# Optimization experiments

Measured on AMD Instinct MI355X. Metric: run time of the kernel, lower is better.

Reference implementation:

```python
import jax, jax.numpy as jnp
import numpy as np
import math

B, C, F, W = 2, 8, 512, 1024
HEADS = 8


def _mcl(x, Wm, b):
    # per-channel linear over feature dim: x (b,c,g,w), Wm (c,f,g), b (c,f)
    return jnp.einsum('bcgw,cfg->bcfw', x, Wm) + b[None, :, :, None]


def _conv(x, w, b, pad):
    y = jax.lax.conv_general_dilated(
        x, w, window_strides=(1, 1), padding=[(0, 0), (pad, pad)],
        dimension_numbers=('NCHW', 'OIHW', 'NCHW'))
    return y + b[None, :, None, None]


def _rope(t):
    # t: (..., seq, d); lucidrains-style interleaved rotary
    d = t.shape[-1]
    seq = t.shape[-2]
    inv_freq = 1.0 / (10000.0 ** (jnp.arange(0, d, 2, dtype=jnp.float32) / d))
    freqs = jnp.arange(seq, dtype=jnp.float32)[:, None] * inv_freq[None, :]  # (seq, d/2)
    emb = jnp.repeat(freqs, 2, axis=-1)  # (seq, d), interleaved f0,f0,f1,f1,...
    cos, sin = jnp.cos(emb), jnp.sin(emb)
    tp = t.reshape(t.shape[:-1] + (d // 2, 2))
    rot = jnp.stack([-tp[..., 1], tp[..., 0]], axis=-1).reshape(t.shape)
    return t * cos.astype(t.dtype) + rot * sin.astype(t.dtype)


def setup_inputs() -> dict:
    key = jax.random.key(0)
    ks = jax.random.split(key, 18)
    s = 0.02
    d = {'x': jax.random.normal(ks[0], (B, C, F, W), dtype=jnp.float32)}
    names = ['q', 'k', 'v', 'o']
    for i, n in enumerate(names):
        d['W' + n] = jax.random.normal(ks[1 + 4 * i], (C, F, F), dtype=jnp.float32) * s
        d['b' + n] = jnp.zeros((C, F), dtype=jnp.float32)
        kw = 7 if n != 'o' else 1
        d[n + '_conv_w'] = jax.random.normal(ks[2 + 4 * i], (C, C, 1, kw), dtype=jnp.float32) * s
        d[n + '_conv_b'] = jnp.zeros((C,), dtype=jnp.float32)
    return d


def reference(x, Wq, bq, q_conv_w, q_conv_b, Wk, bk, k_conv_w, k_conv_b,
              Wv, bv, v_conv_w, v_conv_b, Wo, bo, o_conv_w, o_conv_b):
    b, c, h, w = x.shape
    dh = h // HEADS

    def split_heads(y):  # (b,c,h,w) -> (b,c,heads,w,dh)
        return y.transpose(0, 1, 3, 2).reshape(b, c, w, HEADS, dh).transpose(0, 1, 3, 2, 4)

    q = _rope(split_heads(_conv(_mcl(x, Wq, bq), q_conv_w, q_conv_b, 3)))
    k = _rope(split_heads(_conv(_mcl(x, Wk, bk), k_conv_w, k_conv_b, 3)))
    v = split_heads(_conv(_mcl(x, Wv, bv), v_conv_w, v_conv_b, 3))

    # forced fp32 attention, scaled by sqrt(h) = sqrt(features)
    qk = jnp.einsum('bceqd,bcekd->bceqk', q.astype(jnp.float32), k.astype(jnp.float32)) / math.sqrt(h)
    a = jax.nn.softmax(qk, axis=-1)
    o = jnp.einsum('bceqk,bcekd->bceqd', a, v.astype(jnp.float32))  # (b,c,heads,w,dh)
    o = o.transpose(0, 1, 3, 2, 4).reshape(b, c, w, h).transpose(0, 1, 3, 2)  # (b,c,h,w)

    return _conv(_mcl(o, Wo, bo), o_conv_w, o_conv_b, 0)
```

## Files before the change

kernel.cpp:

```cpp
#include <hip/hip_runtime.h>
#include <hip/hip_bf16.h>
#include <math.h>

#define W_ 1024
#define F_ 512
#define C_ 8
#define B_ 2
#define DH_ 64

typedef __attribute__((ext_vector_type(8))) short short8;
typedef __attribute__((ext_vector_type(4))) short short4v;
typedef __attribute__((ext_vector_type(4))) float f32x4;

__device__ inline unsigned short f2bf(float x) {
    union { float f; unsigned u; } v; v.f = x;
    unsigned r = v.u + 0x7fff + ((v.u >> 16) & 1);
    return (unsigned short)(r >> 16);
}
__device__ inline float bf2f(unsigned short x) {
    union { unsigned u; float f; } v; v.u = (unsigned)x << 16; return v.f;
}

__device__ inline void gll16(const void* g, void* l) {
    __builtin_amdgcn_global_load_lds(
        (const __attribute__((address_space(1))) unsigned int*)g,
        (__attribute__((address_space(3))) unsigned int*)l, 16, 0, 0);
}

__global__ __launch_bounds__(256) void rope_table_kernel(float* __restrict__ cost,
                                                         float* __restrict__ sint) {
    int idx = blockIdx.x * 256 + threadIdx.x;
    if (idx >= W_ * 32) return;
    int w = idx >> 5, i = idx & 31;
    double freq = pow(10000.0, -(double)(2 * i) / 64.0);
    double ang = (double)w * freq;
    cost[idx] = (float)cos(ang);
    sint[idx] = (float)sin(ang);
}

__global__ __launch_bounds__(256) void xt_kernel(
    const float* __restrict__ In, unsigned short* __restrict__ Out)
{
    const int wt = blockIdx.x;
    const int gc = blockIdx.y;
    const int bc = blockIdx.z;
    __shared__ unsigned short T[128][72];
    const int t = threadIdx.x;
    const float* src = In + (size_t)bc * F_ * W_ + (size_t)gc * 64 * W_ + wt * 128;
    const int d0 = (t >> 4) * 4;
    const int w0 = (t & 15) * 4;
    #pragma unroll
    for (int it = 0; it < 2; ++it) {
        int wbase = w0 + it * 64;
        float4 row[4];
        #pragma unroll
        for (int k = 0; k < 4; ++k)
            row[k] = *(const float4*)(src + (size_t)(d0 + k) * W_ + wbase);
        #pragma unroll
        for (int wp = 0; wp < 4; ++wp) {
            ushort4 p;
            p.x = f2bf(((const float*)&row[0])[wp]);
            p.y = f2bf(((const float*)&row[1])[wp]);
            p.z = f2bf(((const float*)&row[2])[wp]);
            p.w = f2bf(((const float*)&row[3])[wp]);
            *(ushort4*)&T[wbase + wp][d0] = p;
        }
    }
    __syncthreads();
    unsigned short* dst = Out + (size_t)bc * W_ * F_ + (size_t)(wt * 128) * F_ + gc * 64;
    const int w = t >> 1, hf = (t & 1) * 32;
    const unsigned short* sr = &T[w][hf];
    uint4* dr = (uint4*)(dst + (size_t)w * F_ + hf);
    dr[0] = ((const uint4*)sr)[0];
    dr[1] = ((const uint4*)sr)[1];
    dr[2] = ((const uint4*)sr)[2];
    dr[3] = ((const uint4*)sr)[3];
}

template<int BF16OUT>
__device__ inline void mcl_body(const unsigned short* Ag, const unsigned short* Bg,
                                const float* biasp, float* Cp, unsigned short* CpB,
                                int f0, int w0)
{
    __shared__ unsigned short As_[128 * 64];
    __shared__ unsigned short Bs_[128 * 64];
    __shared__ float scr[4][16 * 17];

    const int t = threadIdx.x;
    const int wid = t >> 6, lane = t & 63;
    const int l15 = lane & 15, l4 = lane >> 4;
    const int wf = wid >> 1, ww = wid & 1;

    const int grow = lane >> 3;
    const int gcol = ((lane & 7) * 16) ^ ((grow & 7) << 4);

    f32x4 acc[4][4];
    #pragma unroll
    for (int mt = 0; mt < 4; ++mt)
        #pragma unroll
        for (int nt = 0; nt < 4; ++nt) acc[mt][nt] = (f32x4){0.f, 0.f, 0.f, 0.f};

    for (int ks = 0; ks < 8; ++ks) {
        const int k0 = ks * 64;
        __syncthreads();
        #pragma unroll
        for (int i = 0; i < 4; ++i) {
            int rbase = wid * 32 + i * 8;
            int row = rbase + grow;
            gll16(Ag + (size_t)(f0 + row) * F_ + k0 + (gcol >> 1), &As_[rbase * 64]);
            gll16(Bg + (size_t)(w0 + row) * F_ + k0 + (gcol >> 1), &Bs_[rbase * 64]);
        }
        __syncthreads();
        #pragma unroll
        for (int kf = 0; kf < 2; ++kf) {
            short8 af[4], bf_[4];
            #pragma unroll
            for (int mt = 0; mt < 4; ++mt) {
                int row = wf * 64 + mt * 16 + l15;
                int off = (kf * 64 + l4 * 16) ^ ((row & 7) << 4);
                af[mt] = *(const short8*)((const char*)As_ + row * 128 + off);
            }
            #pragma unroll
            for (int nt = 0; nt < 4; ++nt) {
                int row = ww * 64 + nt * 16 + l15;
                int off = (kf * 64 + l4 * 16) ^ ((row & 7) << 4);
                bf_[nt] = *(const short8*)((const char*)Bs_ + row * 128 + off);
            }
            #pragma unroll
            for (int mt = 0; mt < 4; ++mt)
                #pragma unroll
                for (int nt = 0; nt < 4; ++nt)
                    acc[mt][nt] = __builtin_amdgcn_mfma_f32_16x16x32_bf16(af[mt], bf_[nt], acc[mt][nt], 0, 0, 0);
        }
    }

    const float* bp = biasp + f0 + wf * 64;
    float bz[4][4];
    #pragma unroll
    for (int mt = 0; mt < 4; ++mt)
        #pragma unroll
        for (int r = 0; r < 4; ++r) bz[mt][r] = bp[mt * 16 + l4 * 4 + r];

    float* sw = scr[wid];
    #pragma unroll
    for (int mt = 0; mt < 4; ++mt)
        #pragma unroll
        for (int nt = 0; nt < 4; ++nt) {
            #pragma unroll
            for (int r = 0; r < 4; ++r)
                sw[(l4 * 4 + r) * 17 + l15] = acc[mt][nt][r] + bz[mt][r];
            float4 o;
            o.x = sw[l15 * 17 + l4 * 4 + 0];
            o.y = sw[l15 * 17 + l4 * 4 + 1];
            o.z = sw[l15 * 17 + l4 * 4 + 2];
            o.w = sw[l15 * 17 + l4 * 4 + 3];
            size_t off = (size_t)(f0 + wf * 64 + mt * 16 + l15) * W_
                       + w0 + ww * 64 + nt * 16 + l4 * 4;
            if (BF16OUT) {
                ushort4 p;
                p.x = f2bf(o.x); p.y = f2bf(o.y); p.z = f2bf(o.z); p.w = f2bf(o.w);
                *(ushort4*)(CpB + off) = p;
            } else {
                *(float4*)(Cp + off) = o;
            }
        }
}

__global__ __launch_bounds__(256) void mcl_qkv_kernel(
    const unsigned short* __restrict__ Xt,
    const unsigned short* __restrict__ W0, const unsigned short* __restrict__ W1,
    const unsigned short* __restrict__ W2,
    const float* __restrict__ b0, const float* __restrict__ b1, const float* __restrict__ b2,
    unsigned short* __restrict__ Y0, unsigned short* __restrict__ Y1,
    unsigned short* __restrict__ Y2)
{
    const int zz = blockIdx.z;
    const int proj = zz >> 4, bc = zz & 15;
    const int c = bc & 7;
    const unsigned short* Wb = proj == 0 ? W0 : (proj == 1 ? W1 : W2);
    const float* bias = proj == 0 ? b0 : (proj == 1 ? b1 : b2);
    unsigned short* Y = proj == 0 ? Y0 : (proj == 1 ? Y1 : Y2);
    mcl_body<1>(Wb + (size_t)c * F_ * F_, Xt + (size_t)bc * W_ * F_,
                bias + c * F_, nullptr, Y + (size_t)bc * F_ * W_,
                blockIdx.y * 128, blockIdx.x * 128);
}

__global__ __launch_bounds__(256) void mcl_mfma_kernel(
    const unsigned short* __restrict__ Xt, const unsigned short* __restrict__ Wb,
    const float* __restrict__ bias, float* __restrict__ Y)
{
    const int bc = blockIdx.z;
    const int c = bc & 7;
    mcl_body<0>(Wb + (size_t)c * F_ * F_, Xt + (size_t)bc * W_ * F_,
                bias + c * F_, Y + (size_t)bc * F_ * W_, nullptr,
                blockIdx.y * 128, blockIdx.x * 128);
}

__global__ __launch_bounds__(256) void convrope3_kernel(
    unsigned short* __restrict__ Aq, unsigned short* __restrict__ Ak,
    const unsigned short* __restrict__ Av, unsigned short* __restrict__ Vb,
    const float* __restrict__ cwq, const float* __restrict__ cbq,
    const float* __restrict__ cwk, const float* __restrict__ cbk,
    const float* __restrict__ cwv, const float* __restrict__ cbv,
    const float* __restrict__ cost, const float* __restrict__ sint)
{
    const int fp = blockIdx.x;
    const int b = blockIdx.y;
    const int proj = blockIdx.z;
    const unsigned short* In = proj == 0 ? Aq : (proj == 1 ? Ak : Av);
    unsigned short* Yw = proj == 0 ? Aq : (proj == 1 ? Ak : Vb);
    const float* CW = proj == 0 ? cwq : (proj == 1 ? cwk : cwv);
    const float* CB = proj == 0 ? cbq : (proj == 1 ? cbk : cbv);
    const int do_rope = (proj < 2);

    __shared__ unsigned rows[C_][W_];
    __shared__ float wT[C_][7][C_];
    const int t = threadIdx.x;

    #pragma unroll
    for (int ci = 0; ci < 8; ++ci) {
        const unsigned short* s0 = In + ((size_t)(b * C_ + ci) * F_ + 2 * fp) * W_;
        ushort4 a0 = *(const ushort4*)(s0 + t * 4);
        ushort4 a1 = *(const ushort4*)(s0 + W_ + t * 4);
        uint4 p;
        p.x = (unsigned)a0.x | ((unsigned)a1.x << 16);
        p.y = (unsigned)a0.y | ((unsigned)a1.y << 16);
        p.z = (unsigned)a0.z | ((unsigned)a1.z << 16);
        p.w = (unsigned)a0.w | ((unsigned)a1.w << 16);
        *(uint4*)&rows[ci][t * 4] = p;
    }
    for (int idx = t; idx < C_ * C_ * 7; idx += 256) {
        int co = idx & 7; int tmp = idx >> 3; int tt = tmp % 7; int ci = tmp / 7;
        wT[ci][tt][co] = CW[((size_t)co * C_ + ci) * 7 + tt];
    }
    float cb[8];
    #pragma unroll
    for (int co = 0; co < 8; co++) cb[co] = CB[co];
    __syncthreads();

    float acc[4][2][8];
    #pragma unroll
    for (int rep = 0; rep < 4; rep++)
        #pragma unroll
        for (int fi = 0; fi < 2; fi++)
            #pragma unroll
            for (int co = 0; co < 8; co++) acc[rep][fi][co] = cb[co];

    for (int ci = 0; ci < 8; ci++) {
        #pragma unroll
        for (int tt = 0; tt < 7; tt++) {
            float wv[8];
            *(float4*)(wv)     = *(const float4*)&wT[ci][tt][0];
            *(float4*)(wv + 4) = *(const float4*)&wT[ci][tt][4];
            #pragma unroll
            for (int rep = 0; rep < 4; rep++) {
                int ws = t + rep * 256 + tt - 3;
                float v0 = 0.f, v1 = 0.f;
                if ((unsigned)ws < (unsigned)W_) {
                    unsigned pv = rows[ci][ws];
                    union { unsigned u; float f; } c0, c1;
                    c0.u = pv << 16;
                    c1.u = pv & 0xffff0000u;
                    v0 = c0.f;
                    v1 = c1.f;
                }
                #pragma unroll
                for (int co = 0; co < 8; co++) {
                    acc[rep][0][co] = fmaf(v0, wv[co], acc[rep][0][co]);
                    acc[rep][1][co] = fmaf(v1, wv[co], acc[rep][1][co]);
                }
            }
        }
    }
    const int ip = fp & 31;
    #pragma unroll
    for (int rep = 0; rep < 4; rep++) {
        int w = t + rep * 256;
        float c_ = 1.f, s_ = 0.f;
        if (do_rope) { c_ = cost[w * 32 + ip]; s_ = sint[w * 32 + ip]; }
        #pragma unroll
        for (int co = 0; co < 8; co++) {
            float o0 = acc[rep][0][co], o1 = acc[rep][1][co];
            float r0 = do_rope ? (o0 * c_ - o1 * s_) : o0;
            float r1 = do_rope ? (o1 * c_ + o0 * s_) : o1;
            size_t rowb = ((size_t)(b * C_ + co) * F_ + 2 * fp) * W_;
            Yw[rowb + w] = f2bf(r0);
            Yw[rowb + W_ + w] = f2bf(r1);
        }
    }
}

__global__ __launch_bounds__(256) void transpose_qk_kernel(
    const unsigned short* __restrict__ In, unsigned short* __restrict__ Out, float scale)
{
    const int wt = blockIdx.x;
    const int h = blockIdx.y;
    __shared__ unsigned short T[128][72];
    const int t = threadIdx.x;
    const unsigned short* src = In + (size_t)h * 64 * 1024 + wt * 128;
    const int d0 = (t >> 4) * 4;
    const int w0 = (t & 15) * 4;
    #pragma unroll
    for (int it = 0; it < 2; ++it) {
        int wbase = w0 + it * 64;
        ushort4 row[4];
        #pragma unroll
        for (int k = 0; k < 4; ++k)
            row[k] = *(const ushort4*)(src + (size_t)(d0 + k) * 1024 + wbase);
        #pragma unroll
        for (int wp = 0; wp < 4; ++wp) {
            ushort4 p;
            p.x = f2bf(bf2f(((const unsigned short*)&row[0])[wp]) * scale);
            p.y = f2bf(bf2f(((const unsigned short*)&row[1])[wp]) * scale);
            p.z = f2bf(bf2f(((const unsigned short*)&row[2])[wp]) * scale);
            p.w = f2bf(bf2f(((const unsigned short*)&row[3])[wp]) * scale);
            *(ushort4*)&T[wbase + wp][d0] = p;
        }
    }
    __syncthreads();
    unsigned short* dst = Out + ((size_t)h * 1024 + wt * 128) * 64;
    const int w = t >> 1, hf = (t & 1) * 32;
    const unsigned short* sr = &T[w][hf];
    uint4* dr = (uint4*)(dst + w * 64 + hf);
    dr[0] = ((const uint4*)sr)[0];
    dr[1] = ((const uint4*)sr)[1];
    dr[2] = ((const uint4*)sr)[2];
    dr[3] = ((const uint4*)sr)[3];
}

__global__ __launch_bounds__(256) void bf16cvt_kernel(
    const float* __restrict__ In, unsigned short* __restrict__ Out)
{
    size_t i = ((size_t)blockIdx.x * 256 + threadIdx.x) * 8;
    float4 a = *(const float4*)(In + i);
    float4 b = *(const float4*)(In + i + 4);
    ushort4 pa, pb;
    pa.x = f2bf(a.x); pa.y = f2bf(a.y); pa.z = f2bf(a.z); pa.w = f2bf(a.w);
    pb.x = f2bf(b.x); pb.y = f2bf(b.y); pb.z = f2bf(b.z); pb.w = f2bf(b.w);
    *(ushort4*)(Out + i) = pa;
    *(ushort4*)(Out + i + 4) = pb;
}

__global__ __launch_bounds__(256) void attn_mfma_kernel(
    const unsigned short* __restrict__ Qt, const unsigned short* __restrict__ Kt,
    const unsigned short* __restrict__ Vb, unsigned short* __restrict__ Ot)
{
    const int head = blockIdx.x;
    const int qt = blockIdx.y;
    const int t = threadIdx.x;
    const int wid = t >> 6;
    const int lane = t & 63;
    const int l15 = lane & 15;
    const int l4 = lane >> 4;

    __shared__ unsigned short Ks[64 * 64];
    __shared__ unsigned short Vs[64 * 64];
    __shared__ char plds_[4][11264];
    unsigned short* plds = (unsigned short*)plds_[wid];
    float* olds = (float*)plds_[wid];

    const int q0 = qt * 256 + wid * 64;
    const unsigned short* qb = Qt + ((size_t)head * 1024 + q0) * 64;
    const unsigned short* kb = Kt + (size_t)head * 1024 * 64;
    const unsigned short* vb = Vb + (size_t)head * 64 * 1024;

    short8 aq[4][2];
    #pragma unroll
    for (int mt = 0; mt < 4; ++mt)
        #pragma unroll
        for (int kf = 0; kf < 2; ++kf)
            aq[mt][kf] = *(const short8*)(qb + (size_t)(mt * 16 + l15) * 64 + kf * 32 + l4 * 8);

    const int srow = lane >> 3;
    const int schunk = lane & 7;

    f32x4 oa[4][4];
    float li[4] = {0.f, 0.f, 0.f, 0.f};
    #pragma unroll
    for (int mt = 0; mt < 4; ++mt)
        #pragma unroll
        for (int dt = 0; dt < 4; ++dt) oa[mt][dt] = (f32x4){0.f, 0.f, 0.f, 0.f};

    for (int jt = 0; jt < 16; ++jt) {
        const int j0 = jt * 64;
        __syncthreads();
        #pragma unroll
        for (int i = 0; i < 2; ++i) {
            int rbase = wid * 16 + i * 8;
            int row = rbase + srow;
            gll16(kb + (size_t)(j0 + row) * 64 + ((schunk ^ (row & 7)) * 8), &Ks[rbase * 64]);
            gll16(vb + (size_t)row * 1024 + j0 + ((schunk ^ (row & 7)) * 8), &Vs[rbase * 64]);
        }
        __syncthreads();

        #pragma unroll
        for (int nt = 0; nt < 4; ++nt) {
            int row = nt * 16 + l15;
            short8 bk0 = *(const short8*)&Ks[row * 64 + ((l4 ^ (row & 7)) * 8)];
            short8 bk1 = *(const short8*)&Ks[row * 64 + (((4 + l4) ^ (row & 7)) * 8)];
            #pragma unroll
            for (int mt = 0; mt < 4; ++mt) {
                f32x4 a0 = (f32x4){0.f, 0.f, 0.f, 0.f};
                a0 = __builtin_amdgcn_mfma_f32_16x16x32_bf16(bk0, aq[mt][0], a0, 0, 0, 0);
                a0 = __builtin_amdgcn_mfma_f32_16x16x32_bf16(bk1, aq[mt][1], a0, 0, 0, 0);
                float p0 = __builtin_exp2f(a0[0]);
                float p1 = __builtin_exp2f(a0[1]);
                float p2 = __builtin_exp2f(a0[2]);
                float p3 = __builtin_exp2f(a0[3]);
                li[mt] += (p0 + p1) + (p2 + p3);
                union { __hip_bfloat162 h2[2]; short4v s4; } pk;
                pk.h2[0] = __float22bfloat162_rn(make_float2(p0, p1));
                pk.h2[1] = __float22bfloat162_rn(make_float2(p2, p3));
                *(short4v*)(plds + (size_t)(mt * 16 + l15) * 88 + nt * 16 + l4 * 4) = pk.s4;
            }
        }
        short8 pa[4][2];
        #pragma unroll
        for (int mt = 0; mt < 4; ++mt)
            #pragma unroll
            for (int kf = 0; kf < 2; ++kf)
                pa[mt][kf] = *(const short8*)(plds + (size_t)(mt * 16 + l15) * 88 + kf * 32 + l4 * 8);
        #pragma unroll
        for (int dt = 0; dt < 4; ++dt) {
            int row = dt * 16 + l15;
            short8 bv0 = *(const short8*)&Vs[row * 64 + ((l4 ^ (row & 7)) * 8)];
            short8 bv1 = *(const short8*)&Vs[row * 64 + (((4 + l4) ^ (row & 7)) * 8)];
            #pragma unroll
            for (int mt = 0; mt < 4; ++mt) {
                oa[mt][dt] = __builtin_amdgcn_mfma_f32_16x16x32_bf16(pa[mt][0], bv0, oa[mt][dt], 0, 0, 0);
                oa[mt][dt] = __builtin_amdgcn_mfma_f32_16x16x32_bf16(pa[mt][1], bv1, oa[mt][dt], 0, 0, 0);
            }
        }
    }

    float invq[4][4];
    #pragma unroll
    for (int mt = 0; mt < 4; ++mt) {
        float l = li[mt];
        l += __shfl_xor(l, 16);
        l += __shfl_xor(l, 32);
        float inv = 1.f / l;
        #pragma unroll
        for (int r = 0; r < 4; ++r)
            invq[mt][r] = __shfl(inv, l4 * 4 + r);
    }

    #pragma unroll
    for (int mt = 0; mt < 4; ++mt) {
        #pragma unroll
        for (int dt = 0; dt < 4; ++dt)
            #pragma unroll
            for (int r = 0; r < 4; ++r)
                olds[(size_t)(l4 * 4 + r) * 68 + dt * 16 + l15] = oa[mt][dt][r] * invq[mt][r];
        const int ql = lane >> 2, hf = (lane & 3) * 16;
        const float* srow_ = olds + (size_t)ql * 68 + hf;
        unsigned short* dst = Ot + ((size_t)(head >> 3) * W_ + q0 + mt * 16 + ql) * F_
                                 + (head & 7) * 64 + hf;
        short8 pk0, pk1;
        #pragma unroll
        for (int e = 0; e < 8; ++e) { pk0[e] = (short)f2bf(srow_[e]); pk1[e] = (short)f2bf(srow_[8 + e]); }
        *(short8*)(dst) = pk0;
        *(short8*)(dst + 8) = pk1;
    }
}

__global__ __launch_bounds__(256) void oconv_kernel(
    const float* __restrict__ In, const float* __restrict__ OW,
    const float* __restrict__ OB, float* __restrict__ Out)
{
    size_t idx = (size_t)blockIdx.x * 256 + threadIdx.x;
    int b = (int)(idx >> 19);
    size_t fw = idx & (((size_t)1 << 19) - 1);
    const float* in = In + (size_t)b * C_ * F_ * W_ + fw;
    float* out = Out + (size_t)b * C_ * F_ * W_ + fw;
    float v[8];
    #pragma unroll
    for (int ci = 0; ci < 8; ci++) v[ci] = in[(size_t)ci * F_ * W_];
    #pragma unroll
    for (int co = 0; co < 8; co++) {
        float acc = OB[co];
        #pragma unroll
        for (int ci = 0; ci < 8; ci++) acc = fmaf(v[ci], OW[co * 8 + ci], acc);
        out[(size_t)co * F_ * W_] = acc;
    }
}

extern "C" void kernel_launch(void* const* d_in, const int* in_sizes, int n_in,
                              void* d_out, int out_size, void* d_ws, size_t ws_size,
                              hipStream_t stream) {
    const float* x   = (const float*)d_in[0];
    const float* Wq  = (const float*)d_in[1];
    const float* bq  = (const float*)d_in[2];
    const float* qcw = (const float*)d_in[3];
    const float* qcb = (const float*)d_in[4];
    const float* Wk  = (const float*)d_in[5];
    const float* bk  = (const float*)d_in[6];
    const float* kcw = (const float*)d_in[7];
    const float* kcb = (const float*)d_in[8];
    const float* Wv  = (const float*)d_in[9];
    const float* bv  = (const float*)d_in[10];
    const float* vcw = (const float*)d_in[11];
    const float* vcb = (const float*)d_in[12];
    const float* Wo  = (const float*)d_in[13];
    const float* bo  = (const float*)d_in[14];
    const float* ocw = (const float*)d_in[15];
    const float* ocb = (const float*)d_in[16];

    float* ws = (float*)d_ws;
    const size_t SZ = (size_t)B_ * C_ * F_ * W_;
    const size_t WSF = (size_t)C_ * F_ * F_ / 2;
    unsigned short* Aq = (unsigned short*)ws;
    unsigned short* Ak = (unsigned short*)(ws + SZ);
    unsigned short* Av = (unsigned short*)(ws + 2 * SZ);
    unsigned short* XtVb = (unsigned short*)(ws + 3 * SZ);
    unsigned short* WqB = (unsigned short*)(ws + 3 * SZ + SZ / 2);
    unsigned short* WkB = (unsigned short*)(ws + 3 * SZ + SZ / 2 + 2 * WSF);
    unsigned short* WvB = (unsigned short*)(ws + 3 * SZ + SZ / 2 + 4 * WSF);
    unsigned short* WoB = (unsigned short*)(ws + 3 * SZ + SZ / 2 + 6 * WSF);
    unsigned short* Qt  = (unsigned short*)(ws + 2 * SZ);
    unsigned short* Kt  = Qt + SZ;
    unsigned short* Ot  = (unsigned short*)ws;
    float* Ao = ws + SZ;
    float* cost = ws + 4 * SZ;
    float* sint = cost + (size_t)W_ * 32;

    const float qscale = (float)(1.4426950408889634 / 22.627416997969522);

    rope_table_kernel<<<(W_ * 32 + 255) / 256, 256, 0, stream>>>(cost, sint);
    xt_kernel<<<dim3(8, 8, 16), 256, 0, stream>>>(x, XtVb);
    bf16cvt_kernel<<<1024, 256, 0, stream>>>(Wq, WqB);
    bf16cvt_kernel<<<1024, 256, 0, stream>>>(Wk, WkB);
    bf16cvt_kernel<<<1024, 256, 0, stream>>>(Wv, WvB);
    bf16cvt_kernel<<<1024, 256, 0, stream>>>(Wo, WoB);

    mcl_qkv_kernel<<<dim3(8, 4, 48), 256, 0, stream>>>(
        XtVb, WqB, WkB, WvB, bq, bk, bv, Aq, Ak, Av);

    convrope3_kernel<<<dim3(F_ / 2, B_, 3), 256, 0, stream>>>(
        Aq, Ak, Av, XtVb, qcw, qcb, kcw, kcb, vcw, vcb, cost, sint);

    transpose_qk_kernel<<<dim3(W_ / 128, 128), 256, 0, stream>>>(Aq, Qt, qscale);
    transpose_qk_kernel<<<dim3(W_ / 128, 128), 256, 0, stream>>>(Ak, Kt, 1.0f);

    attn_mfma_kernel<<<dim3(128, 4), 256, 0, stream>>>(Qt, Kt, XtVb, Ot);

    mcl_mfma_kernel<<<dim3(8, 4, 16), 256, 0, stream>>>(Ot, WoB, bo, Ao);
    oconv_kernel<<<(B_ * F_ * W_) / 256, 256, 0, stream>>>(Ao, ocw, ocb, (float*)d_out);
}
```

Measured before the change: 262.2 us.

## Split conv+rope kernel across width chunks with halo and out-of-place output

```diff
diff --git a/kernel.cpp b/kernel.cpp
--- a/kernel.cpp
+++ b/kernel.cpp
@@ -196,38 +196,46 @@
                 blockIdx.y * 128, blockIdx.x * 128);
 }
 
-__global__ __launch_bounds__(256) void convrope3_kernel(
-    unsigned short* __restrict__ Aq, unsigned short* __restrict__ Ak,
-    const unsigned short* __restrict__ Av, unsigned short* __restrict__ Vb,
+__global__ __launch_bounds__(256) void convrope_w2_kernel(
+    const unsigned short* __restrict__ Aq, const unsigned short* __restrict__ Ak,
+    const unsigned short* __restrict__ Av,
+    unsigned short* __restrict__ Cq, unsigned short* __restrict__ Ck,
+    unsigned short* __restrict__ Vb,
     const float* __restrict__ cwq, const float* __restrict__ cbq,
     const float* __restrict__ cwk, const float* __restrict__ cbk,
     const float* __restrict__ cwv, const float* __restrict__ cbv,
     const float* __restrict__ cost, const float* __restrict__ sint)
 {
-    const int fp = blockIdx.x;
-    const int b = blockIdx.y;
-    const int proj = blockIdx.z;
+    const int wc = blockIdx.x;
+    const int fp = blockIdx.y;
+    const int proj = blockIdx.z >> 1;
+    const int b = blockIdx.z & 1;
     const unsigned short* In = proj == 0 ? Aq : (proj == 1 ? Ak : Av);
-    unsigned short* Yw = proj == 0 ? Aq : (proj == 1 ? Ak : Vb);
+    unsigned short* Out = proj == 0 ? Cq : (proj == 1 ? Ck : Vb);
     const float* CW = proj == 0 ? cwq : (proj == 1 ? cwk : cwv);
     const float* CB = proj == 0 ? cbq : (proj == 1 ? cbk : cbv);
     const int do_rope = (proj < 2);
 
-    __shared__ unsigned rows[C_][W_];
+    __shared__ unsigned rows[C_][264];
     __shared__ float wT[C_][7][C_];
     const int t = threadIdx.x;
+    const int w0 = wc * 256;
 
     #pragma unroll
     for (int ci = 0; ci < 8; ++ci) {
         const unsigned short* s0 = In + ((size_t)(b * C_ + ci) * F_ + 2 * fp) * W_;
-        ushort4 a0 = *(const ushort4*)(s0 + t * 4);
-        ushort4 a1 = *(const ushort4*)(s0 + W_ + t * 4);
-        uint4 p;
-        p.x = (unsigned)a0.x | ((unsigned)a1.x << 16);
-        p.y = (unsigned)a0.y | ((unsigned)a1.y << 16);
-        p.z = (unsigned)a0.z | ((unsigned)a1.z << 16);
-        p.w = (unsigned)a0.w | ((unsigned)a1.w << 16);
-        *(uint4*)&rows[ci][t * 4] = p;
+        int gw = w0 + t - 3;
+        unsigned v = 0;
+        if ((unsigned)gw < (unsigned)W_)
+            v = (unsigned)s0[gw] | ((unsigned)s0[W_ + gw] << 16);
+        rows[ci][t] = v;
+        if (t < 8) {
+            int gw2 = w0 + 256 + t - 3;
+            unsigned v2 = 0;
+            if ((unsigned)gw2 < (unsigned)W_)
+                v2 = (unsigned)s0[gw2] | ((unsigned)s0[W_ + gw2] << 16);
+            rows[ci][256 + t] = v2;
+        }
     }
     for (int idx = t; idx < C_ * C_ * 7; idx += 256) {
         int co = idx & 7; int tmp = idx >> 3; int tt = tmp % 7; int ci = tmp / 7;
@@ -238,55 +246,41 @@
     for (int co = 0; co < 8; co++) cb[co] = CB[co];
     __syncthreads();
 
-    float acc[4][2][8];
-    #pragma unroll
-    for (int rep = 0; rep < 4; rep++)
-        #pragma unroll
-        for (int fi = 0; fi < 2; fi++)
-            #pragma unroll
-            for (int co = 0; co < 8; co++) acc[rep][fi][co] = cb[co];
-
-    for (int ci = 0; ci < 8; ci++) {
-        #pragma unroll
-        for (int tt = 0; tt < 7; tt++) {
+    float acc0[8], acc1[8];
+    #pragma unroll
+    for (int co = 0; co < 8; ++co) { acc0[co] = cb[co]; acc1[co] = cb[co]; }
+
+    #pragma unroll 1
+    for (int ci = 0; ci < 8; ++ci) {
+        #pragma unroll
+        for (int tt = 0; tt < 7; ++tt) {
             float wv[8];
             *(float4*)(wv)     = *(const float4*)&wT[ci][tt][0];
             *(float4*)(wv + 4) = *(const float4*)&wT[ci][tt][4];
-            #pragma unroll
-            for (int rep = 0; rep < 4; rep++) {
-                int ws = t + rep * 256 + tt - 3;
-                float v0 = 0.f, v1 = 0.f;
-                if ((unsigned)ws < (unsigned)W_) {
-                    unsigned pv = rows[ci][ws];
-                    union { unsigned u; float f; } c0, c1;
-                    c0.u = pv << 16;
-                    c1.u = pv & 0xffff0000u;
-                    v0 = c0.f;
-                    v1 = c1.f;
-                }
-                #pragma unroll
-                for (int co = 0; co < 8; co++) {
-                    acc[rep][0][co] = fmaf(v0, wv[co], acc[rep][0][co]);
-                    acc[rep][1][co] = fmaf(v1, wv[co], acc[rep][1][co]);
-                }
+            unsigned pv = rows[ci][t + tt];
+            union { unsigned u; float f; } c0, c1;
+            c0.u = pv << 16;
+            c1.u = pv & 0xffff0000u;
+            #pragma unroll
+            for (int co = 0; co < 8; ++co) {
+                acc0[co] = fmaf(c0.f, wv[co], acc0[co]);
+                acc1[co] = fmaf(c1.f, wv[co], acc1[co]);
             }
         }
     }
+
     const int ip = fp & 31;
-    #pragma unroll
-    for (int rep = 0; rep < 4; rep++) {
-        int w = t + rep * 256;
-        float c_ = 1.f, s_ = 0.f;
-        if (do_rope) { c_ = cost[w * 32 + ip]; s_ = sint[w * 32 + ip]; }
-        #pragma unroll
-        for (int co = 0; co < 8; co++) {
-            float o0 = acc[rep][0][co], o1 = acc[rep][1][co];
-            float r0 = do_rope ? (o0 * c_ - o1 * s_) : o0;
-            float r1 = do_rope ? (o1 * c_ + o0 * s_) : o1;
-            size_t rowb = ((size_t)(b * C_ + co) * F_ + 2 * fp) * W_;
-            Yw[rowb + w] = f2bf(r0);
-            Yw[rowb + W_ + w] = f2bf(r1);
-        }
+    const int w = w0 + t;
+    float c_ = 1.f, s_ = 0.f;
+    if (do_rope) { c_ = cost[w * 32 + ip]; s_ = sint[w * 32 + ip]; }
+    #pragma unroll
+    for (int co = 0; co < 8; ++co) {
+        float o0 = acc0[co], o1 = acc1[co];
+        float r0 = do_rope ? (o0 * c_ - o1 * s_) : o0;
+        float r1 = do_rope ? (o1 * c_ + o0 * s_) : o1;
+        size_t rowb = ((size_t)(b * C_ + co) * F_ + 2 * fp) * W_;
+        Out[rowb + w] = f2bf(r0);
+        Out[rowb + W_ + w] = f2bf(r1);
     }
 }
 
@@ -510,7 +504,9 @@
     const size_t SZ = (size_t)B_ * C_ * F_ * W_;
     const size_t WSF = (size_t)C_ * F_ * F_ / 2;
     unsigned short* Aq = (unsigned short*)ws;
+    unsigned short* Cq = Aq + SZ;
     unsigned short* Ak = (unsigned short*)(ws + SZ);
+    unsigned short* Ck = Ak + SZ;
     unsigned short* Av = (unsigned short*)(ws + 2 * SZ);
     unsigned short* XtVb = (unsigned short*)(ws + 3 * SZ);
     unsigned short* WqB = (unsigned short*)(ws + 3 * SZ + SZ / 2);
@@ -536,11 +532,12 @@
     mcl_qkv_kernel<<<dim3(8, 4, 48), 256, 0, stream>>>(
         XtVb, WqB, WkB, WvB, bq, bk, bv, Aq, Ak, Av);
 
-    convrope3_kernel<<<dim3(F_ / 2, B_, 3), 256, 0, stream>>>(
-        Aq, Ak, Av, XtVb, qcw, qcb, kcw, kcb, vcw, vcb, cost, sint);
-
-    transpose_qk_kernel<<<dim3(W_ / 128, 128), 256, 0, stream>>>(Aq, Qt, qscale);
-    transpose_qk_kernel<<<dim3(W_ / 128, 128), 256, 0, stream>>>(Ak, Kt, 1.0f);
+    convrope_w2_kernel<<<dim3(4, F_ / 2, 6), 256, 0, stream>>>(
+        Aq, Ak, Av, Cq, Ck, XtVb,
+        qcw, qcb, kcw, kcb, vcw, vcb, cost, sint);
+
+    transpose_qk_kernel<<<dim3(W_ / 128, 128), 256, 0, stream>>>(Cq, Qt, qscale);
+    transpose_qk_kernel<<<dim3(W_ / 128, 128), 256, 0, stream>>>(Ck, Kt, 1.0f);
 
     attn_mfma_kernel<<<dim3(128, 4), 256, 0, stream>>>(Qt, Kt, XtVb, Ot);
 
```

Measured after the change: 247.6 us. 1.06x faster.
